# Kernel optimization log

Measured on AMD Instinct MI355X. Metric: run time of the kernel, lower is better.

## Reference

```python
import jax, jax.numpy as jnp
import numpy as np

B, C, H, W = 8, 16, 64, 64
D, N = 1, 512  # embedding_dim, num_embeddings


def setup_inputs() -> dict:
    key = jax.random.key(0)
    k1, k2 = jax.random.split(key)
    x = jax.random.normal(k1, (B, C, H, W), dtype=jnp.float32)
    weight = jax.random.uniform(k2, (D, N), dtype=jnp.float32)  # torch.rand init
    return {"x": x, "weight": weight}


def reference(x, weight):
    b, c, h, w = x.shape
    # dist: [B,C,H,W,N] via broadcast (D==1), argmin over codebook axis
    dist = (x[..., None] - weight) ** 2
    argmin = jnp.argmin(dist, axis=-1)  # [B,C,H,W] int
    # faithful replication of index_select + view([B,H,W,C]) + permute(0,3,1,2)
    codes = jnp.take(weight.T, argmin.reshape(-1), axis=0)  # [B*C*H*W, 1]
    quantized = codes.reshape(b, h, w, c).transpose(0, 3, 1, 2)  # [B,C,H,W]
    e_latent_loss = jnp.mean((x - jax.lax.stop_gradient(quantized)) ** 2)
    q_latent_loss = jnp.mean((quantized - jax.lax.stop_gradient(x)) ** 2)
    # straight-through estimator
    quantized_st = x + jax.lax.stop_gradient(quantized - x)
    return quantized_st, q_latent_loss, e_latent_loss
```

## Files before the change

### kernel.cpp

```cpp
#include <hip/hip_runtime.h>
#include <hip/hip_bf16.h>


#define E_TOTAL 524288
#define NCODE   512
#define BLOCK   256
#define NBLOCKS (E_TOTAL / BLOCK)

__global__ __launch_bounds__(BLOCK) void vq_main_kernel(
    const float* __restrict__ x, const float* __restrict__ wt,
    float* __restrict__ out, double* __restrict__ partial) {
  __shared__ float lw[NCODE];
  __shared__ double lsum[BLOCK / 64];

  const int t = threadIdx.x;
  for (int k = t; k < NCODE; k += BLOCK) lw[k] = wt[k];
  __syncthreads();

  const int o = blockIdx.x * BLOCK + t;
  const int w = o & 63;
  const int h = (o >> 6) & 63;
  const int c = (o >> 12) & 15;
  const int b = o >> 16;
  const int ip = b * 65536 + h * 1024 + w * 16 + c;

  const float xq = x[ip];

  unsigned best = 0xFFFFFFFFu;
#pragma unroll 8
  for (int n = 0; n < NCODE; ++n) {
    const float d = xq - lw[n];
    const float d2 = d * d;
    const unsigned key = (__float_as_uint(d2) & 0xFFFFFE00u) | (unsigned)n;
    best = best < key ? best : key;
  }
  const float wq = lw[best & 511u];

  out[o] = wq;

  const float diff = x[o] - wq;
  double ds = (double)diff * (double)diff;

#pragma unroll
  for (int off = 32; off > 0; off >>= 1) ds += __shfl_down(ds, off, 64);
  const int lane = t & 63, wave = t >> 6;
  if (lane == 0) lsum[wave] = ds;
  __syncthreads();
  if (t == 0) {
    double s = 0.0;
#pragma unroll
    for (int i = 0; i < BLOCK / 64; ++i) s += lsum[i];
    partial[blockIdx.x] = s;
  }
}

__global__ __launch_bounds__(BLOCK) void vq_reduce_kernel(
    const double* __restrict__ partial, float* __restrict__ out) {
  __shared__ double lsum[BLOCK / 64];
  const int t = threadIdx.x;
  double s = 0.0;
  for (int k = t; k < NBLOCKS; k += BLOCK) s += partial[k];
#pragma unroll
  for (int off = 32; off > 0; off >>= 1) s += __shfl_down(s, off, 64);
  const int lane = t & 63, wave = t >> 6;
  if (lane == 0) lsum[wave] = s;
  __syncthreads();
  if (t == 0) {
    double tot = 0.0;
#pragma unroll
    for (int i = 0; i < BLOCK / 64; ++i) tot += lsum[i];
    const float m = (float)(tot / (double)E_TOTAL);
    out[E_TOTAL] = m;
    out[E_TOTAL + 1] = m;
  }
}

extern "C" void kernel_launch(void* const* d_in, const int* in_sizes, int n_in,
                              void* d_out, int out_size, void* d_ws, size_t ws_size,
                              hipStream_t stream) {
  const float* x = (const float*)d_in[0];
  const float* wt = (const float*)d_in[1];
  float* out = (float*)d_out;
  double* partial = (double*)d_ws;

  vq_main_kernel<<<NBLOCKS, BLOCK, 0, stream>>>(x, wt, out, partial);
  vq_reduce_kernel<<<1, BLOCK, 0, stream>>>(partial, out);
}
```

Baseline: 85.27 us.

## Process four elements per thread with vectorized codebook reads from LDS

Measured after the change: 93.01 us. 9.1% more time.

```diff
diff --git a/kernel.cpp b/kernel.cpp
--- a/kernel.cpp
+++ b/kernel.cpp
@@ -5,41 +5,68 @@
 #define E_TOTAL 524288
 #define NCODE   512
 #define BLOCK   256
-#define NBLOCKS (E_TOTAL / BLOCK)
+#define M       4
+#define TOT_THREADS (E_TOTAL / M)
+#define NBLOCKS (TOT_THREADS / BLOCK)
 
 __global__ __launch_bounds__(BLOCK) void vq_main_kernel(
     const float* __restrict__ x, const float* __restrict__ wt,
     float* __restrict__ out, double* __restrict__ partial) {
-  __shared__ float lw[NCODE];
+  __shared__ float4 lw4[NCODE / 4];
   __shared__ double lsum[BLOCK / 64];
 
   const int t = threadIdx.x;
-  for (int k = t; k < NCODE; k += BLOCK) lw[k] = wt[k];
+  if (t < NCODE / 4) lw4[t] = ((const float4*)wt)[t];
   __syncthreads();
 
-  const int o = blockIdx.x * BLOCK + t;
-  const int w = o & 63;
-  const int h = (o >> 6) & 63;
-  const int c = (o >> 12) & 15;
-  const int b = o >> 16;
-  const int ip = b * 65536 + h * 1024 + w * 16 + c;
+  const int tid = blockIdx.x * BLOCK + t;
 
-  const float xq = x[ip];
+  int oo[M];
+  float xq[M];
+  unsigned best[M];
+#pragma unroll
+  for (int m = 0; m < M; ++m) {
+    const int o = tid + m * TOT_THREADS;
+    oo[m] = o;
+    const int w = o & 63;
+    const int h = (o >> 6) & 63;
+    const int c = (o >> 12) & 15;
+    const int b = o >> 16;
+    const int ip = b * 65536 + h * 1024 + w * 16 + c;
+    xq[m] = x[ip];
+    best[m] = 0xFFFFFFFFu;
+  }
 
-  unsigned best = 0xFFFFFFFFu;
-#pragma unroll 8
-  for (int n = 0; n < NCODE; ++n) {
-    const float d = xq - lw[n];
-    const float d2 = d * d;
-    const unsigned key = (__float_as_uint(d2) & 0xFFFFFE00u) | (unsigned)n;
-    best = best < key ? best : key;
+#pragma unroll 4
+  for (int j = 0; j < NCODE / 4; ++j) {
+    const float4 wv = lw4[j];
+    const unsigned n0 = 4u * (unsigned)j;
+#pragma unroll
+    for (int m = 0; m < M; ++m) {
+      float d0 = xq[m] - wv.x; float e0 = d0 * d0;
+      float d1 = xq[m] - wv.y; float e1 = d1 * d1;
+      float d2 = xq[m] - wv.z; float e2 = d2 * d2;
+      float d3 = xq[m] - wv.w; float e3 = d3 * d3;
+      unsigned k0 = (__float_as_uint(e0) & 0xFFFFFE00u) | (n0 + 0u);
+      unsigned k1 = (__float_as_uint(e1) & 0xFFFFFE00u) | (n0 + 1u);
+      unsigned k2 = (__float_as_uint(e2) & 0xFFFFFE00u) | (n0 + 2u);
+      unsigned k3 = (__float_as_uint(e3) & 0xFFFFFE00u) | (n0 + 3u);
+      unsigned a = k0 < k1 ? k0 : k1;
+      unsigned b2 = k2 < k3 ? k2 : k3;
+      a = a < b2 ? a : b2;
+      best[m] = best[m] < a ? best[m] : a;
+    }
   }
-  const float wq = lw[best & 511u];
 
-  out[o] = wq;
-
-  const float diff = x[o] - wq;
-  double ds = (double)diff * (double)diff;
+  const float* lw = (const float*)lw4;
+  double ds = 0.0;
+#pragma unroll
+  for (int m = 0; m < M; ++m) {
+    const float wq = lw[best[m] & 511u];
+    out[oo[m]] = wq;
+    const float diff = x[oo[m]] - wq;
+    ds += (double)diff * (double)diff;
+  }
 
 #pragma unroll
   for (int off = 32; off > 0; off >>= 1) ds += __shfl_down(ds, off, 64);
```

## Sort codebook once and replace linear argmin with binary search

Applied to the files above, without the earlier changes.

New measurement: 79.48 us. -6.8%, faster.

```diff
diff --git a/kernel.cpp b/kernel.cpp
--- a/kernel.cpp
+++ b/kernel.cpp
@@ -7,14 +7,30 @@
 #define BLOCK   256
 #define NBLOCKS (E_TOTAL / BLOCK)
 
+__global__ __launch_bounds__(NCODE) void vq_prep_kernel(
+    const float* __restrict__ wt, float* __restrict__ sorted) {
+  __shared__ float lw[NCODE];
+  const int t = threadIdx.x;
+  lw[t] = wt[t];
+  __syncthreads();
+  const float v = lw[t];
+  int r = 0;
+  for (int n = 0; n < NCODE; ++n) {
+    const float u = lw[n];
+    r += (u < v || (u == v && n < t)) ? 1 : 0;
+  }
+  sorted[r] = v;
+}
+
 __global__ __launch_bounds__(BLOCK) void vq_main_kernel(
-    const float* __restrict__ x, const float* __restrict__ wt,
+    const float* __restrict__ x, const float* __restrict__ sorted,
     float* __restrict__ out, double* __restrict__ partial) {
-  __shared__ float lw[NCODE];
+  __shared__ float ls[NCODE + 2];
   __shared__ double lsum[BLOCK / 64];
 
   const int t = threadIdx.x;
-  for (int k = t; k < NCODE; k += BLOCK) lw[k] = wt[k];
+  for (int k = t; k < NCODE; k += BLOCK) ls[k + 1] = sorted[k];
+  if (t == 0) { ls[0] = -3.0e38f; ls[NCODE + 1] = 3.0e38f; }
   __syncthreads();
 
   const int o = blockIdx.x * BLOCK + t;
@@ -23,18 +39,19 @@
   const int c = (o >> 12) & 15;
   const int b = o >> 16;
   const int ip = b * 65536 + h * 1024 + w * 16 + c;
+  const float xv = x[ip];
 
-  const float xq = x[ip];
-
-  unsigned best = 0xFFFFFFFFu;
-#pragma unroll 8
-  for (int n = 0; n < NCODE; ++n) {
-    const float d = xq - lw[n];
-    const float d2 = d * d;
-    const unsigned key = (__float_as_uint(d2) & 0xFFFFFE00u) | (unsigned)n;
-    best = best < key ? best : key;
+  unsigned idx = 0;
+#pragma unroll
+  for (unsigned step = NCODE / 2; step; step >>= 1) {
+    const float sv = ls[idx + step];
+    idx = (sv <= xv) ? idx + step : idx;
   }
-  const float wq = lw[best & 511u];
+  const float left = ls[idx];
+  const float right = ls[idx + 1];
+  const float dl = xv - left;  const float d2l = dl * dl;
+  const float dr = xv - right; const float d2r = dr * dr;
+  const float wq = (d2l <= d2r) ? left : right;
 
   out[o] = wq;
 
@@ -81,8 +98,10 @@
   const float* x = (const float*)d_in[0];
   const float* wt = (const float*)d_in[1];
   float* out = (float*)d_out;
-  double* partial = (double*)d_ws;
+  float* sorted = (float*)d_ws;
+  double* partial = (double*)((char*)d_ws + 4096);
 
-  vq_main_kernel<<<NBLOCKS, BLOCK, 0, stream>>>(x, wt, out, partial);
+  vq_prep_kernel<<<1, NCODE, 0, stream>>>(wt, sorted);
+  vq_main_kernel<<<NBLOCKS, BLOCK, 0, stream>>>(x, sorted, out, partial);
   vq_reduce_kernel<<<1, BLOCK, 0, stream>>>(partial, out);
 }
```
